# Kernel tuning notes

Measured on AMD Instinct MI355X. Metric: run time of the kernel, lower is better.

Reference implementation:

```python
import jax, jax.numpy as jnp
import numpy as np

NUM_EXPERTS = 8


def _ffn(x, w1, b1, w2, b2):
    # x: [T, H]; w1: [8H, H]; w2: [H, 4H]
    gu = x @ w1.T + b1                      # [T, 8H]
    gate, up = jnp.split(gu, 2, axis=-1)    # each [T, 4H]
    h = jax.nn.gelu(gate, approximate=True) * up
    return h @ w2.T + b2                    # [T, H]


def setup_inputs() -> dict:
    key = jax.random.key(0)
    ks = jax.random.split(key, 4)
    H, E, F = 1024, NUM_EXPERTS, 4096
    scale = 0.02
    return {
        "x": jax.random.normal(ks[0], (4, 1024, H), dtype=jnp.float32),
        "gate_w": jax.random.normal(ks[1], (E, H), dtype=jnp.float32) * scale,
        "gate_b": jnp.zeros((E,), dtype=jnp.float32),
        "w1": jax.random.normal(ks[2], (E, 2 * F, H), dtype=jnp.float32) * scale,
        "b1": jnp.zeros((E, 2 * F), dtype=jnp.float32),
        "w2": jax.random.normal(ks[3], (E, H, F), dtype=jnp.float32) * scale,
        "b2": jnp.zeros((E, H), dtype=jnp.float32),
    }


def reference(x, gate_w, gate_b, w1, b1, w2, b2):
    B, S, H = x.shape
    E = gate_w.shape[0]
    T = B * S
    xf = x.reshape(T, H)

    logits = xf @ gate_w.T + gate_b          # [T, E]
    probs = jax.nn.softmax(logits, axis=-1)
    vals, idx = jax.lax.top_k(probs, 2)      # [T, 2]

    # load balancing loss (matches torch bincount of top-1 expert)
    top1_onehot = jax.nn.one_hot(idx[:, 0], E, dtype=jnp.float32)
    frequencies = top1_onehot.sum(0) / T
    probability = probs.mean(0)
    load_balancing_loss = (probability * frequencies).mean() * float(E * E)

    # normalize top-2 scores
    total = vals.sum(axis=-1, keepdims=True)
    norm_scores = vals / total               # [T, 2]

    # per-token per-expert combine weights [T, E]
    weights = (jax.nn.one_hot(idx[:, 0], E, dtype=xf.dtype) * norm_scores[:, 0:1]
               + jax.nn.one_hot(idx[:, 1], E, dtype=xf.dtype) * norm_scores[:, 1:2])

    out = jnp.zeros_like(xf)
    for e in range(E):  # fixed small loop over experts
        out = out + weights[:, e:e + 1] * _ffn(xf, w1[e], b1[e], w2[e], b2[e])

    return out.reshape(B, S, H), load_balancing_loss
```

## Files before the change

kernel.cpp:

```cpp
#include <hip/hip_runtime.h>

#define T_TOK 4096
#define HDIM 1024
#define FDIM 4096
#define NEXP 8
#define ROWCAP 9216
#define NTILES_MAX 72

typedef __attribute__((ext_vector_type(8))) short short8;
typedef __attribute__((ext_vector_type(4))) float f32x4;

__device__ __forceinline__ unsigned short f2bf(float f) {
    unsigned int u = __builtin_bit_cast(unsigned int, f);
    u += 0x7fffu + ((u >> 16) & 1u);
    return (unsigned short)(u >> 16);
}

__device__ __forceinline__ float gelu_tanh(float x) {
    const float k0 = 0.7978845608028654f;
    return 0.5f * x * (1.0f + tanhf(k0 * (x + 0.044715f * x * x * x)));
}

__global__ __launch_bounds__(256) void routing_kernel(
    const float* __restrict__ x, const float* __restrict__ gate_w,
    const float* __restrict__ gate_b,
    int* __restrict__ tokTop1, int* __restrict__ tokE,
    float* __restrict__ tokW, float* __restrict__ tokProbs)
{
    __shared__ float gws[NEXP * HDIM];
    int tid = threadIdx.x;
    for (int i = tid; i < NEXP * HDIM / 4; i += 256)
        ((float4*)gws)[i] = ((const float4*)gate_w)[i];
    __syncthreads();
    int lane = tid & 63;
    int t = blockIdx.x * 4 + (tid >> 6);
    float acc[NEXP];
    #pragma unroll
    for (int e = 0; e < NEXP; e++) acc[e] = 0.f;
    const float* xr = x + (size_t)t * HDIM;
    for (int k = lane; k < HDIM; k += 64) {
        float xv = xr[k];
        #pragma unroll
        for (int e = 0; e < NEXP; e++) acc[e] += xv * gws[e * HDIM + k];
    }
    #pragma unroll
    for (int e = 0; e < NEXP; e++) {
        #pragma unroll
        for (int off = 32; off >= 1; off >>= 1)
            acc[e] += __shfl_xor(acc[e], off);
    }
    if (lane == 0) {
        float m = -1e30f;
        #pragma unroll
        for (int e = 0; e < NEXP; e++) { acc[e] += gate_b[e]; m = fmaxf(m, acc[e]); }
        float p[NEXP]; float s = 0.f;
        #pragma unroll
        for (int e = 0; e < NEXP; e++) { p[e] = __expf(acc[e] - m); s += p[e]; }
        float inv = 1.f / s;
        int i0 = -1; float v0 = -1.f;
        #pragma unroll
        for (int e = 0; e < NEXP; e++) {
            p[e] *= inv;
            tokProbs[t * NEXP + e] = p[e];
            if (p[e] > v0) { v0 = p[e]; i0 = e; }
        }
        int i1 = -1; float v1 = -1.f;
        #pragma unroll
        for (int e = 0; e < NEXP; e++)
            if (e != i0 && p[e] > v1) { v1 = p[e]; i1 = e; }
        float tot = v0 + v1;
        tokTop1[t] = i0;
        tokE[2 * t] = i0; tokE[2 * t + 1] = i1;
        tokW[2 * t] = v0 / tot; tokW[2 * t + 1] = v1 / tot;
    }
}

__global__ __launch_bounds__(256) void stats_kernel(
    const int* __restrict__ tokTop1, const int* __restrict__ tokE,
    const float* __restrict__ tokProbs,
    int* __restrict__ counts, int* __restrict__ cnt1, float* __restrict__ probSum)
{
    int e = blockIdx.x, tid = threadIdx.x;
    float ps = 0.f; int c1 = 0, c = 0;
    for (int t = tid; t < T_TOK; t += 256) {
        ps += tokProbs[t * NEXP + e];
        c1 += (tokTop1[t] == e);
        c  += (tokE[2 * t] == e) + (tokE[2 * t + 1] == e);
    }
    __shared__ float sps[256]; __shared__ int sc1[256]; __shared__ int sc[256];
    sps[tid] = ps; sc1[tid] = c1; sc[tid] = c; __syncthreads();
    for (int s = 128; s > 0; s >>= 1) {
        if (tid < s) { sps[tid] += sps[tid + s]; sc1[tid] += sc1[tid + s]; sc[tid] += sc[tid + s]; }
        __syncthreads();
    }
    if (tid == 0) { probSum[e] = sps[0]; cnt1[e] = sc1[0]; counts[e] = sc[0]; }
}

__global__ void scan_loss_kernel(
    const int* __restrict__ counts, const int* __restrict__ cnt1,
    const float* __restrict__ probSum,
    int* __restrict__ offsets, int* __restrict__ cursor,
    int* __restrict__ tileE, int* __restrict__ nTiles,
    float* __restrict__ loss_out)
{
    int off = 0, nt = 0; float loss = 0.f;
    for (int e = 0; e < NEXP; e++) {
        offsets[e] = off;
        int pt = (counts[e] + 127) >> 7;
        for (int i = 0; i < pt; i++) tileE[nt++] = e;
        off += pt * 128;
        cursor[e] = 0;
        loss += probSum[e] * (float)cnt1[e];
    }
    nTiles[0] = nt;
    nTiles[1] = off;
    *loss_out = loss * 8.0f / ((float)T_TOK * (float)T_TOK);
}

__global__ __launch_bounds__(256) void assign_kernel(
    const int* __restrict__ tokE, const float* __restrict__ tokW,
    const int* __restrict__ offsets, int* __restrict__ cursor,
    int* __restrict__ rowTok, float* __restrict__ rowW)
{
    int t = blockIdx.x * 256 + threadIdx.x;
    #pragma unroll
    for (int s = 0; s < 2; s++) {
        int e = tokE[2 * t + s];
        int pos = atomicAdd(&cursor[e], 1);
        int row = offsets[e] + pos;
        rowTok[row] = t;
        rowW[row] = tokW[2 * t + s];
    }
}

__global__ __launch_bounds__(256) void convertw_kernel(
    const float* __restrict__ src, unsigned short* __restrict__ dst, long n8)
{
    long stride = (long)gridDim.x * 256;
    for (long i = (long)blockIdx.x * 256 + threadIdx.x; i < n8; i += stride) {
        const float4* s = (const float4*)src + 2 * i;
        float4 f0 = s[0], f1 = s[1];
        uint4 pk;
        pk.x = (unsigned)f2bf(f0.x) | ((unsigned)f2bf(f0.y) << 16);
        pk.y = (unsigned)f2bf(f0.z) | ((unsigned)f2bf(f0.w) << 16);
        pk.z = (unsigned)f2bf(f1.x) | ((unsigned)f2bf(f1.y) << 16);
        pk.w = (unsigned)f2bf(f1.z) | ((unsigned)f2bf(f1.w) << 16);
        ((uint4*)dst)[i] = pk;
    }
}

__global__ __launch_bounds__(256) void gather_kernel(
    const float* __restrict__ x, const int* __restrict__ rowTok,
    const int* __restrict__ offsets, const int* __restrict__ counts,
    const int* __restrict__ tileE, const int* __restrict__ nTiles,
    int chunkBase, unsigned short* __restrict__ Xc)
{
    int gr = chunkBase + blockIdx.x;
    if (gr >= nTiles[1]) return;
    int tid = threadIdx.x;
    int e = tileE[gr >> 7];
    ushort4* dst = (ushort4*)(Xc + (size_t)(gr - chunkBase) * HDIM);
    if (gr - offsets[e] < counts[e]) {
        int t = rowTok[gr];
        float4 v = ((const float4*)(x + (size_t)t * HDIM))[tid];
        ushort4 b;
        b.x = f2bf(v.x); b.y = f2bf(v.y); b.z = f2bf(v.z); b.w = f2bf(v.w);
        dst[tid] = b;
    } else {
        ushort4 z; z.x = 0; z.y = 0; z.z = 0; z.w = 0;
        dst[tid] = z;
    }
}

__global__ __launch_bounds__(256) void bias_out_kernel(
    const float* __restrict__ b2, const int* __restrict__ tokE,
    const float* __restrict__ tokW, float* __restrict__ out)
{
    int t = blockIdx.x, tid = threadIdx.x;
    int e0 = tokE[2 * t], e1 = tokE[2 * t + 1];
    float w0 = tokW[2 * t], w1 = tokW[2 * t + 1];
    float4 a = ((const float4*)(b2 + (size_t)e0 * HDIM))[tid];
    float4 b = ((const float4*)(b2 + (size_t)e1 * HDIM))[tid];
    float4 r;
    r.x = w0 * a.x + w1 * b.x; r.y = w0 * a.y + w1 * b.y;
    r.z = w0 * a.z + w1 * b.z; r.w = w0 * a.w + w1 * b.w;
    ((float4*)(out + (size_t)t * HDIM))[tid] = r;
}

template<bool WB>
__global__ __launch_bounds__(256) void gemm1_kernel(
    const unsigned short* __restrict__ Xc, const void* __restrict__ w1,
    const float* __restrict__ b1, const int* __restrict__ tileE,
    const int* __restrict__ nTiles, int chunkBase,
    unsigned short* __restrict__ hc)
{
    int gt = (chunkBase >> 7) + blockIdx.y;
    if (gt >= nTiles[0]) return;
    int e = tileE[gt];
    int localBase = gt * 128 - chunkBase;
    int cTile = blockIdx.x;

    __shared__ unsigned short As[128 * 72];
    __shared__ unsigned short Bs[128 * 72];

    int tid = threadIdx.x;
    int lane = tid & 63, wave = tid >> 6;
    int wm = wave & 1, wn = wave >> 1;
    int q = lane >> 4, c15 = lane & 15;

    const float* w1e_f = nullptr;
    const unsigned short* w1e_h = nullptr;
    if constexpr (WB) w1e_h = (const unsigned short*)w1 + (size_t)e * (2 * FDIM) * HDIM;
    else              w1e_f = (const float*)w1 + (size_t)e * (2 * FDIM) * HDIM;

    f32x4 accG[4][2], accU[4][2];
    #pragma unroll
    for (int a = 0; a < 4; a++)
        #pragma unroll
        for (int b = 0; b < 2; b++)
            #pragma unroll
            for (int c = 0; c < 4; c++) { accG[a][b][c] = 0.f; accU[a][b][c] = 0.f; }

    for (int k0 = 0; k0 < HDIM; k0 += 64) {
        __syncthreads();
        #pragma unroll
        for (int ci = 0; ci < 4; ci++) {
            int chunk = tid + 256 * ci;
            int i = chunk >> 3, kc = chunk & 7;
            uint4 av = *(const uint4*)(Xc + (size_t)(localBase + i) * HDIM + k0 + kc * 8);
            *(uint4*)(As + i * 72 + kc * 8) = av;
        }
        #pragma unroll
        for (int ci = 0; ci < 4; ci++) {
            int chunk = tid + 256 * ci;
            int j = chunk >> 3, kc = chunk & 7;
            int w1row = (j < 64) ? (cTile * 64 + j) : (FDIM + cTile * 64 + j - 64);
            if constexpr (WB) {
                uint4 pk = *(const uint4*)(w1e_h + (size_t)w1row * HDIM + k0 + kc * 8);
                *(uint4*)(Bs + j * 72 + kc * 8) = pk;
            } else {
                const float* src = w1e_f + (size_t)w1row * HDIM + k0 + kc * 8;
                float4 f0 = *(const float4*)src;
                float4 f1 = *(const float4*)(src + 4);
                uint4 pk;
                pk.x = (unsigned)f2bf(f0.x) | ((unsigned)f2bf(f0.y) << 16);
                pk.y = (unsigned)f2bf(f0.z) | ((unsigned)f2bf(f0.w) << 16);
                pk.z = (unsigned)f2bf(f1.x) | ((unsigned)f2bf(f1.y) << 16);
                pk.w = (unsigned)f2bf(f1.z) | ((unsigned)f2bf(f1.w) << 16);
                *(uint4*)(Bs + j * 72 + kc * 8) = pk;
            }
        }
        __syncthreads();
        #pragma unroll
        for (int kk = 0; kk < 64; kk += 32) {
            short8 aF[4], bG[2], bU[2];
            #pragma unroll
            for (int mi = 0; mi < 4; mi++)
                aF[mi] = *(const short8*)(As + (wm * 64 + mi * 16 + c15) * 72 + kk + q * 8);
            #pragma unroll
            for (int ni = 0; ni < 2; ni++) {
                bG[ni] = *(const short8*)(Bs + (wn * 32 + ni * 16 + c15) * 72 + kk + q * 8);
                bU[ni] = *(const short8*)(Bs + (64 + wn * 32 + ni * 16 + c15) * 72 + kk + q * 8);
            }
            #pragma unroll
            for (int mi = 0; mi < 4; mi++)
                #pragma unroll
                for (int ni = 0; ni < 2; ni++) {
                    accG[mi][ni] = __builtin_amdgcn_mfma_f32_16x16x32_bf16(aF[mi], bG[ni], accG[mi][ni], 0, 0, 0);
                    accU[mi][ni] = __builtin_amdgcn_mfma_f32_16x16x32_bf16(aF[mi], bU[ni], accU[mi][ni], 0, 0, 0);
                }
        }
    }
    const float* b1e = b1 + (size_t)e * (2 * FDIM);
    #pragma unroll
    for (int mi = 0; mi < 4; mi++)
        #pragma unroll
        for (int ni = 0; ni < 2; ni++) {
            int hcol = cTile * 64 + wn * 32 + ni * 16 + c15;
            float bg = b1e[hcol], bu = b1e[FDIM + hcol];
            #pragma unroll
            for (int r = 0; r < 4; r++) {
                int row = wm * 64 + mi * 16 + q * 4 + r;
                float g = accG[mi][ni][r] + bg;
                float u = accU[mi][ni][r] + bu;
                hc[(size_t)(localBase + row) * FDIM + hcol] = f2bf(gelu_tanh(g) * u);
            }
        }
}

template<bool WB>
__global__ __launch_bounds__(256) void gemm2_kernel(
    const unsigned short* __restrict__ hc, const void* __restrict__ w2,
    const int* __restrict__ offsets, const int* __restrict__ counts,
    const int* __restrict__ rowTok, const float* __restrict__ rowW,
    const int* __restrict__ tileE, const int* __restrict__ nTiles,
    int chunkBase, float* __restrict__ out)
{
    int gt = (chunkBase >> 7) + blockIdx.y;
    if (gt >= nTiles[0]) return;
    int e = tileE[gt];
    int localBase = gt * 128 - chunkBase;
    int rowBaseG = gt * 128;
    int cTile = blockIdx.x;

    __shared__ unsigned short As[128 * 72];
    __shared__ unsigned short Bs[128 * 72];

    int tid = threadIdx.x;
    int lane = tid & 63, wave = tid >> 6;
    int wm = wave & 1, wn = wave >> 1;
    int q = lane >> 4, c15 = lane & 15;

    const float* w2e_f = nullptr;
    const unsigned short* w2e_h = nullptr;
    if constexpr (WB) w2e_h = (const unsigned short*)w2 + (size_t)e * HDIM * FDIM;
    else              w2e_f = (const float*)w2 + (size_t)e * HDIM * FDIM;

    f32x4 acc[4][4];
    #pragma unroll
    for (int a = 0; a < 4; a++)
        #pragma unroll
        for (int b = 0; b < 4; b++)
            #pragma unroll
            for (int c = 0; c < 4; c++) acc[a][b][c] = 0.f;

    for (int k0 = 0; k0 < FDIM; k0 += 64) {
        __syncthreads();
        #pragma unroll
        for (int ci = 0; ci < 4; ci++) {
            int chunk = tid + 256 * ci;
            int i = chunk >> 3, kc = chunk & 7;
            uint4 av = *(const uint4*)(hc + (size_t)(localBase + i) * FDIM + k0 + kc * 8);
            *(uint4*)(As + i * 72 + kc * 8) = av;
        }
        #pragma unroll
        for (int ci = 0; ci < 4; ci++) {
            int chunk = tid + 256 * ci;
            int j = chunk >> 3, kc = chunk & 7;
            if constexpr (WB) {
                uint4 pk = *(const uint4*)(w2e_h + (size_t)(cTile * 128 + j) * FDIM + k0 + kc * 8);
                *(uint4*)(Bs + j * 72 + kc * 8) = pk;
            } else {
                const float* src = w2e_f + (size_t)(cTile * 128 + j) * FDIM + k0 + kc * 8;
                float4 f0 = *(const float4*)src;
                float4 f1 = *(const float4*)(src + 4);
                uint4 pk;
                pk.x = (unsigned)f2bf(f0.x) | ((unsigned)f2bf(f0.y) << 16);
                pk.y = (unsigned)f2bf(f0.z) | ((unsigned)f2bf(f0.w) << 16);
                pk.z = (unsigned)f2bf(f1.x) | ((unsigned)f2bf(f1.y) << 16);
                pk.w = (unsigned)f2bf(f1.z) | ((unsigned)f2bf(f1.w) << 16);
                *(uint4*)(Bs + j * 72 + kc * 8) = pk;
            }
        }
        __syncthreads();
        #pragma unroll
        for (int kk = 0; kk < 64; kk += 32) {
            short8 aF[4], bF[4];
            #pragma unroll
            for (int mi = 0; mi < 4; mi++)
                aF[mi] = *(const short8*)(As + (wm * 64 + mi * 16 + c15) * 72 + kk + q * 8);
            #pragma unroll
            for (int ni = 0; ni < 4; ni++)
                bF[ni] = *(const short8*)(Bs + (wn * 64 + ni * 16 + c15) * 72 + kk + q * 8);
            #pragma unroll
            for (int mi = 0; mi < 4; mi++)
                #pragma unroll
                for (int ni = 0; ni < 4; ni++)
                    acc[mi][ni] = __builtin_amdgcn_mfma_f32_16x16x32_bf16(aF[mi], bF[ni], acc[mi][ni], 0, 0, 0);
        }
    }
    #pragma unroll
    for (int mi = 0; mi < 4; mi++) {
        #pragma unroll
        for (int r = 0; r < 4; r++) {
            int row = wm * 64 + mi * 16 + q * 4 + r;
            int grow = rowBaseG + row;
            if (grow - offsets[e] < counts[e]) {
                int t = rowTok[grow];
                float w = rowW[grow];
                float* od = out + (size_t)t * HDIM + cTile * 128 + wn * 64 + c15;
                #pragma unroll
                for (int ni = 0; ni < 4; ni++)
                    atomicAdd(od + ni * 16, w * acc[mi][ni][r]);
            }
        }
    }
}

extern "C" void kernel_launch(void* const* d_in, const int* in_sizes, int n_in,
                              void* d_out, int out_size, void* d_ws, size_t ws_size,
                              hipStream_t stream) {
    (void)in_sizes; (void)n_in; (void)out_size;
    const float* x      = (const float*)d_in[0];
    const float* gate_w = (const float*)d_in[1];
    const float* gate_b = (const float*)d_in[2];
    const float* w1     = (const float*)d_in[3];
    const float* b1     = (const float*)d_in[4];
    const float* w2     = (const float*)d_in[5];
    const float* b2     = (const float*)d_in[6];
    float* out = (float*)d_out;

    char* ws = (char*)d_ws;
    int*   counts   = (int*)(ws + 0);
    int*   cnt1     = (int*)(ws + 32);
    int*   cursor   = (int*)(ws + 64);
    int*   offsets  = (int*)(ws + 96);
    float* probSum  = (float*)(ws + 128);
    int*   nTiles   = (int*)(ws + 160);
    int*   tileE    = (int*)(ws + 256);
    int*   tokTop1  = (int*)(ws + 1024);
    int*   tokE     = (int*)(ws + 1024 + 16384);
    float* tokW     = (float*)(ws + 1024 + 49152);
    float* tokProbs = (float*)(ws + 1024 + 81920);
    int*   rowTok   = (int*)(ws + 1024 + 212992);
    float* rowW     = (float*)(ws + 1024 + 249856);
    const size_t fixedEnd = 512 * 1024;

    const size_t W1E = (size_t)NEXP * 2 * FDIM * HDIM;
    const size_t W2E = (size_t)NEXP * HDIM * FDIM;
    const size_t WBYTES = (W1E + W2E) * 2;
    bool wbf16 = ws_size >= fixedEnd + WBYTES + (size_t)128 * (HDIM + FDIM) * 2;

    unsigned short* w1b = nullptr;
    unsigned short* w2b = nullptr;
    size_t chunkStart = fixedEnd;
    if (wbf16) {
        w1b = (unsigned short*)(ws + fixedEnd);
        w2b = w1b + W1E;
        chunkStart = fixedEnd + WBYTES;
    }

    size_t avail = ws_size > chunkStart ? ws_size - chunkStart : 0;
    int ch = (int)((avail / (10240ULL * 128ULL)) * 128ULL);
    if (ch > ROWCAP) ch = ROWCAP;
    if (ch < 128) ch = 128;
    unsigned short* Xc = (unsigned short*)(ws + chunkStart);
    unsigned short* hc = (unsigned short*)(ws + chunkStart + (size_t)ch * HDIM * 2);
    int nChunks = (ROWCAP + ch - 1) / ch;

    if (wbf16) {
        convertw_kernel<<<2048, 256, 0, stream>>>(w1, w1b, (long)(W1E / 8));
        convertw_kernel<<<2048, 256, 0, stream>>>(w2, w2b, (long)(W2E / 8));
    }

    routing_kernel<<<T_TOK / 4, 256, 0, stream>>>(x, gate_w, gate_b, tokTop1, tokE, tokW, tokProbs);
    stats_kernel<<<NEXP, 256, 0, stream>>>(tokTop1, tokE, tokProbs, counts, cnt1, probSum);
    scan_loss_kernel<<<1, 1, 0, stream>>>(counts, cnt1, probSum, offsets, cursor, tileE, nTiles,
                                          out + (size_t)T_TOK * HDIM);
    assign_kernel<<<T_TOK / 256, 256, 0, stream>>>(tokE, tokW, offsets, cursor, rowTok, rowW);
    bias_out_kernel<<<T_TOK, 256, 0, stream>>>(b2, tokE, tokW, out);

    for (int c = 0; c < nChunks; c++) {
        int base = c * ch;
        int rows = ROWCAP - base; if (rows > ch) rows = ch;
        int tiles = rows >> 7;
        gather_kernel<<<rows, 256, 0, stream>>>(x, rowTok, offsets, counts, tileE, nTiles, base, Xc);
        if (wbf16) {
            gemm1_kernel<true><<<dim3(FDIM / 64, tiles), 256, 0, stream>>>(
                Xc, (const void*)w1b, b1, tileE, nTiles, base, hc);
            gemm2_kernel<true><<<dim3(HDIM / 128, tiles), 256, 0, stream>>>(
                hc, (const void*)w2b, offsets, counts, rowTok, rowW, tileE, nTiles, base, out);
        } else {
            gemm1_kernel<false><<<dim3(FDIM / 64, tiles), 256, 0, stream>>>(
                Xc, (const void*)w1, b1, tileE, nTiles, base, hc);
            gemm2_kernel<false><<<dim3(HDIM / 128, tiles), 256, 0, stream>>>(
                hc, (const void*)w2, offsets, counts, rowTok, rowW, tileE, nTiles, base, out);
        }
    }
}
```

Measured before the change: 1.011 ms.

## Load GEMM tiles directly into LDS with XOR-swizzled layout and cheaper GELU

Replaces register-staged global-to-LDS copies in both expert GEMMs with direct global_load_lds 16-byte transfers, for the bf16-weight path. The padded 72-stride shared tiles become unpadded 64-stride tiles with an XOR swizzle to avoid bank conflicts. Fragment reads are remapped to match. GELU's tanh is rewritten as an equivalent sigmoid form using __expf. This cuts VGPR staging and instruction overhead in the load phase, but depends on the direct-to-LDS lane layout matching the swizzle exactly.

```diff
diff --git a/kernel.cpp b/kernel.cpp
--- a/kernel.cpp
+++ b/kernel.cpp
@@ -17,8 +17,14 @@
 }
 
 __device__ __forceinline__ float gelu_tanh(float x) {
-    const float k0 = 0.7978845608028654f;
-    return 0.5f * x * (1.0f + tanhf(k0 * (x + 0.044715f * x * x * x)));
+    float z = 1.5957691216057308f * (x + 0.044715f * x * x * x);
+    return x / (1.0f + __expf(-z));
+}
+
+__device__ __forceinline__ void gload16(const unsigned short* g, unsigned short* l) {
+    __builtin_amdgcn_global_load_lds(
+        (const __attribute__((address_space(1))) unsigned int*)g,
+        (__attribute__((address_space(3))) unsigned int*)l, 16, 0, 0);
 }
 
 __global__ __launch_bounds__(256) void routing_kernel(
@@ -200,16 +206,16 @@
     int localBase = gt * 128 - chunkBase;
     int cTile = blockIdx.x;
 
-    __shared__ unsigned short As[128 * 72];
-    __shared__ unsigned short Bs[128 * 72];
+    __shared__ unsigned short As[128 * 64];
+    __shared__ unsigned short Bs[128 * 64];
 
     int tid = threadIdx.x;
     int lane = tid & 63, wave = tid >> 6;
     int wm = wave & 1, wn = wave >> 1;
     int q = lane >> 4, c15 = lane & 15;
 
+    const unsigned short* w1e_h = nullptr;
     const float* w1e_f = nullptr;
-    const unsigned short* w1e_h = nullptr;
     if constexpr (WB) w1e_h = (const unsigned short*)w1 + (size_t)e * (2 * FDIM) * HDIM;
     else              w1e_f = (const float*)w1 + (size_t)e * (2 * FDIM) * HDIM;
 
@@ -223,22 +229,37 @@
 
     for (int k0 = 0; k0 < HDIM; k0 += 64) {
         __syncthreads();
-        #pragma unroll
-        for (int ci = 0; ci < 4; ci++) {
-            int chunk = tid + 256 * ci;
-            int i = chunk >> 3, kc = chunk & 7;
-            uint4 av = *(const uint4*)(Xc + (size_t)(localBase + i) * HDIM + k0 + kc * 8);
-            *(uint4*)(As + i * 72 + kc * 8) = av;
-        }
-        #pragma unroll
-        for (int ci = 0; ci < 4; ci++) {
-            int chunk = tid + 256 * ci;
-            int j = chunk >> 3, kc = chunk & 7;
-            int w1row = (j < 64) ? (cTile * 64 + j) : (FDIM + cTile * 64 + j - 64);
-            if constexpr (WB) {
-                uint4 pk = *(const uint4*)(w1e_h + (size_t)w1row * HDIM + k0 + kc * 8);
-                *(uint4*)(Bs + j * 72 + kc * 8) = pk;
-            } else {
+        if constexpr (WB) {
+            #pragma unroll
+            for (int ci = 0; ci < 4; ci++) {
+                int G = ci * 256 + wave * 64 + lane;
+                int row = G >> 3;
+                int gs = (lane & 7) ^ (row & 7);
+                gload16(Xc + (size_t)(localBase + row) * HDIM + k0 + gs * 8,
+                        As + (ci * 256 + wave * 64) * 8);
+            }
+            #pragma unroll
+            for (int ci = 0; ci < 4; ci++) {
+                int G = ci * 256 + wave * 64 + lane;
+                int j = G >> 3;
+                int gs = (lane & 7) ^ (j & 7);
+                int w1row = (j < 64) ? (cTile * 64 + j) : (FDIM + cTile * 64 + (j - 64));
+                gload16(w1e_h + (size_t)w1row * HDIM + k0 + gs * 8,
+                        Bs + (ci * 256 + wave * 64) * 8);
+            }
+        } else {
+            #pragma unroll
+            for (int ci = 0; ci < 4; ci++) {
+                int chunk = tid + 256 * ci;
+                int i = chunk >> 3, kc = chunk & 7;
+                uint4 av = *(const uint4*)(Xc + (size_t)(localBase + i) * HDIM + k0 + kc * 8);
+                *(uint4*)(As + i * 64 + ((kc ^ (i & 7)) * 8)) = av;
+            }
+            #pragma unroll
+            for (int ci = 0; ci < 4; ci++) {
+                int chunk = tid + 256 * ci;
+                int j = chunk >> 3, kc = chunk & 7;
+                int w1row = (j < 64) ? (cTile * 64 + j) : (FDIM + cTile * 64 + (j - 64));
                 const float* src = w1e_f + (size_t)w1row * HDIM + k0 + kc * 8;
                 float4 f0 = *(const float4*)src;
                 float4 f1 = *(const float4*)(src + 4);
@@ -247,20 +268,21 @@
                 pk.y = (unsigned)f2bf(f0.z) | ((unsigned)f2bf(f0.w) << 16);
                 pk.z = (unsigned)f2bf(f1.x) | ((unsigned)f2bf(f1.y) << 16);
                 pk.w = (unsigned)f2bf(f1.z) | ((unsigned)f2bf(f1.w) << 16);
-                *(uint4*)(Bs + j * 72 + kc * 8) = pk;
+                *(uint4*)(Bs + j * 64 + ((kc ^ (j & 7)) * 8)) = pk;
             }
         }
         __syncthreads();
         #pragma unroll
         for (int kk = 0; kk < 64; kk += 32) {
+            int slot = (((q + (kk >> 3)) ^ (c15 & 7)) & 7) * 8;
             short8 aF[4], bG[2], bU[2];
             #pragma unroll
             for (int mi = 0; mi < 4; mi++)
-                aF[mi] = *(const short8*)(As + (wm * 64 + mi * 16 + c15) * 72 + kk + q * 8);
+                aF[mi] = *(const short8*)(As + (wm * 64 + mi * 16 + c15) * 64 + slot);
             #pragma unroll
             for (int ni = 0; ni < 2; ni++) {
-                bG[ni] = *(const short8*)(Bs + (wn * 32 + ni * 16 + c15) * 72 + kk + q * 8);
-                bU[ni] = *(const short8*)(Bs + (64 + wn * 32 + ni * 16 + c15) * 72 + kk + q * 8);
+                bG[ni] = *(const short8*)(Bs + (wn * 32 + ni * 16 + c15) * 64 + slot);
+                bU[ni] = *(const short8*)(Bs + (64 + wn * 32 + ni * 16 + c15) * 64 + slot);
             }
             #pragma unroll
             for (int mi = 0; mi < 4; mi++)
@@ -303,16 +325,16 @@
     int rowBaseG = gt * 128;
     int cTile = blockIdx.x;
 
-    __shared__ unsigned short As[128 * 72];
-    __shared__ unsigned short Bs[128 * 72];
+    __shared__ unsigned short As[128 * 64];
+    __shared__ unsigned short Bs[128 * 64];
 
     int tid = threadIdx.x;
     int lane = tid & 63, wave = tid >> 6;
     int wm = wave & 1, wn = wave >> 1;
     int q = lane >> 4, c15 = lane & 15;
 
+    const unsigned short* w2e_h = nullptr;
     const float* w2e_f = nullptr;
-    const unsigned short* w2e_h = nullptr;
     if constexpr (WB) w2e_h = (const unsigned short*)w2 + (size_t)e * HDIM * FDIM;
     else              w2e_f = (const float*)w2 + (size_t)e * HDIM * FDIM;
 
@@ -326,21 +348,35 @@
 
     for (int k0 = 0; k0 < FDIM; k0 += 64) {
         __syncthreads();
-        #pragma unroll
-        for (int ci = 0; ci < 4; ci++) {
-            int chunk = tid + 256 * ci;
-            int i = chunk >> 3, kc = chunk & 7;
-            uint4 av = *(const uint4*)(hc + (size_t)(localBase + i) * FDIM + k0 + kc * 8);
-            *(uint4*)(As + i * 72 + kc * 8) = av;
-        }
-        #pragma unroll
-        for (int ci = 0; ci < 4; ci++) {
-            int chunk = tid + 256 * ci;
-            int j = chunk >> 3, kc = chunk & 7;
-            if constexpr (WB) {
-                uint4 pk = *(const uint4*)(w2e_h + (size_t)(cTile * 128 + j) * FDIM + k0 + kc * 8);
-                *(uint4*)(Bs + j * 72 + kc * 8) = pk;
-            } else {
+        if constexpr (WB) {
+            #pragma unroll
+            for (int ci = 0; ci < 4; ci++) {
+                int G = ci * 256 + wave * 64 + lane;
+                int row = G >> 3;
+                int gs = (lane & 7) ^ (row & 7);
+                gload16(hc + (size_t)(localBase + row) * FDIM + k0 + gs * 8,
+                        As + (ci * 256 + wave * 64) * 8);
+            }
+            #pragma unroll
+            for (int ci = 0; ci < 4; ci++) {
+                int G = ci * 256 + wave * 64 + lane;
+                int j = G >> 3;
+                int gs = (lane & 7) ^ (j & 7);
+                gload16(w2e_h + (size_t)(cTile * 128 + j) * FDIM + k0 + gs * 8,
+                        Bs + (ci * 256 + wave * 64) * 8);
+            }
+        } else {
+            #pragma unroll
+            for (int ci = 0; ci < 4; ci++) {
+                int chunk = tid + 256 * ci;
+                int i = chunk >> 3, kc = chunk & 7;
+                uint4 av = *(const uint4*)(hc + (size_t)(localBase + i) * FDIM + k0 + kc * 8);
+                *(uint4*)(As + i * 64 + ((kc ^ (i & 7)) * 8)) = av;
+            }
+            #pragma unroll
+            for (int ci = 0; ci < 4; ci++) {
+                int chunk = tid + 256 * ci;
+                int j = chunk >> 3, kc = chunk & 7;
                 const float* src = w2e_f + (size_t)(cTile * 128 + j) * FDIM + k0 + kc * 8;
                 float4 f0 = *(const float4*)src;
                 float4 f1 = *(const float4*)(src + 4);
@@ -349,19 +385,20 @@
                 pk.y = (unsigned)f2bf(f0.z) | ((unsigned)f2bf(f0.w) << 16);
                 pk.z = (unsigned)f2bf(f1.x) | ((unsigned)f2bf(f1.y) << 16);
                 pk.w = (unsigned)f2bf(f1.z) | ((unsigned)f2bf(f1.w) << 16);
-                *(uint4*)(Bs + j * 72 + kc * 8) = pk;
+                *(uint4*)(Bs + j * 64 + ((kc ^ (j & 7)) * 8)) = pk;
             }
         }
         __syncthreads();
         #pragma unroll
         for (int kk = 0; kk < 64; kk += 32) {
+            int slot = (((q + (kk >> 3)) ^ (c15 & 7)) & 7) * 8;
             short8 aF[4], bF[4];
             #pragma unroll
             for (int mi = 0; mi < 4; mi++)
-                aF[mi] = *(const short8*)(As + (wm * 64 + mi * 16 + c15) * 72 + kk + q * 8);
+                aF[mi] = *(const short8*)(As + (wm * 64 + mi * 16 + c15) * 64 + slot);
             #pragma unroll
             for (int ni = 0; ni < 4; ni++)
-                bF[ni] = *(const short8*)(Bs + (wn * 64 + ni * 16 + c15) * 72 + kk + q * 8);
+                bF[ni] = *(const short8*)(Bs + (wn * 64 + ni * 16 + c15) * 64 + slot);
             #pragma unroll
             for (int mi = 0; mi < 4; mi++)
                 #pragma unroll
```

Result: faster. 986.2 us (-2.5%).
